# Kernel optimization log

Measured on AMD Instinct MI355X. Metric: run time of the kernel, lower is better.

Reference implementation:

```python
import jax, jax.numpy as jnp
import numpy as np

LAMBDA = 0.1   # lambda_ init arg
RHO = 1.0      # ADMM penalty parameter
N_ITERS = 50   # fixed ADMM iteration count (replaces eps_rel/eps_abs stopping rule, jit-friendly)


def _admm_box_qp(Q1, P):
    """Solve, for every (b, n): min_x 0.5 x^T Q1[b] x + P[b,n]^T x  s.t. 0 <= x <= 1.
    Q1: [b, m, m] (shared across n, so factor once per b), P: [b, n, m]. Returns z: [b, n, m]."""
    b, n, m = P.shape
    M_inv = jnp.linalg.inv(Q1 + RHO * jnp.eye(m, dtype=Q1.dtype))  # [b, m, m]

    x0 = jnp.zeros((b, n, m), P.dtype)

    def step(carry, _):
        x, z, u = carry
        rhs = RHO * (z - u) - P                       # [b, n, m]
        x = jnp.einsum('bij,bnj->bni', M_inv, rhs)    # x-update: (Q1 + rho I) x = rhs
        z = jnp.clip(x + u, 0.0, 1.0)                 # z-update: projection onto box [lb, ub] = [0, 1]
        u = u + x - z                                 # dual update
        return (x, z, u), None

    (x, z, u), _ = jax.lax.scan(step, (x0, x0, x0), None, length=N_ITERS)
    return z


def reference(Q, V):
    b, n, d = Q.shape
    m = V.shape[1]
    V = V / m
    # Q1 = 2 V V^T : [b, m, m]
    Q1 = 2.0 * jnp.einsum('bmd,bkd->bmk', V, V)
    # P = -2 V Q^T + lambda/m : [b, n, m]  (avoid materializing the b*n stacked copies of Q1)
    P = -2.0 * jnp.einsum('bmd,bnd->bnm', V, Q) + LAMBDA / m
    x = _admm_box_qp(Q1, P)                           # [b, n, m] in [0, 1]
    xb = jnp.where(x > 0.5, 1.0, 0.0)                 # hard threshold
    coeffs = xb / (jnp.abs(xb).sum(axis=-1, keepdims=True) + 1e-10)
    return jnp.einsum('bnm,bmd->bnd', coeffs, V)


def setup_inputs() -> dict:
    key = jax.random.key(0)
    kq, kv = jax.random.split(key)
    Q = jax.random.normal(kq, (8, 2048, 128), dtype=jnp.float32)
    V = jax.random.normal(kv, (8, 128, 128), dtype=jnp.float32)
    return {"Q": Q, "V": V}
```

## Files before the change

### kernel.cpp

```cpp
#include <hip/hip_runtime.h>

#define NROWS 2048
#define MDIM 128
#define NITER 50
#define PSTR 65
#define RSTR 136
#define XSTR 132

#define RH0_B 0
#define RM0_B 17408
#define RH1_B 34816
#define RM1_B 52224
#define BUF_STRIDE 34816
#define WM_B 69632
#define CNT_B 104448
#define SMEM_BYTES 108544
#define QST_B 0
#define PMAT_B 33792
#define XB_B 0
#define CF_B 33792

typedef unsigned short ushort_t;
typedef __attribute__((ext_vector_type(8))) _Float16 f16x8;
typedef __attribute__((ext_vector_type(8))) unsigned short us8;
typedef __attribute__((ext_vector_type(4))) unsigned short us4;
typedef __attribute__((ext_vector_type(4))) float f32x4;

__global__ __launch_bounds__(256) void mk_m64(const float* __restrict__ V,
                                              double* __restrict__ M,
                                              double* __restrict__ X0,
                                              double* __restrict__ vs) {
  __shared__ double sA[16][130];
  __shared__ double sB[32][130];
  const int b = blockIdx.x >> 5, t = blockIdx.x & 31;
  const int i0 = (t >> 2) << 4, j0 = (t & 3) << 5;
  const float* Vb = V + b * MDIM * MDIM;
  const int tid = threadIdx.x;
  const double S = 1.0 / 128.0;
  for (int idx = tid; idx < 512; idx += 256) {
    const int r = idx >> 5, c4 = (idx & 31) << 2;
    float4 v = *(const float4*)(Vb + (i0 + r) * MDIM + c4);
    sA[r][c4 + 0] = v.x * S; sA[r][c4 + 1] = v.y * S;
    sA[r][c4 + 2] = v.z * S; sA[r][c4 + 3] = v.w * S;
  }
  for (int idx = tid; idx < 1024; idx += 256) {
    const int r = idx >> 5, c4 = (idx & 31) << 2;
    float4 w = *(const float4*)(Vb + (j0 + r) * MDIM + c4);
    sB[r][c4 + 0] = w.x * S; sB[r][c4 + 1] = w.y * S;
    sB[r][c4 + 2] = w.z * S; sB[r][c4 + 3] = w.w * S;
  }
  if (vs) {
    double* Tb = vs + b * 16384;
    const int base2 = t * 512;
    for (int k = tid; k < 512; k += 256) {
      const int idx = base2 + k;
      const int j = idx >> 7, c = idx & 127;
      Tb[idx] = (double)Vb[c * 128 + j] * (1.0 / 128.0);
    }
  }
  __syncthreads();
  const int tx = tid & 15, ty = tid >> 4;
  double acc0 = 0.0, acc1 = 0.0;
  for (int k = 0; k < 128; ++k) {
    const double a0 = sA[ty][k];
    const double b0 = sB[tx * 2 + 0][k], b1 = sB[tx * 2 + 1][k];
    acc0 = fma(a0, b0, acc0); acc1 = fma(a0, b1, acc1);
  }
  double* Mb = M + b * 16384;
  double* Xb = X0 + b * 16384;
#pragma unroll
  for (int j = 0; j < 2; ++j) {
    const int gi = i0 + ty, gj = j0 + tx * 2 + j;
    const double diag = (gi == gj) ? 1.0 : 0.0;
    const double mv = 2.0 * (j ? acc1 : acc0) + diag;
    Mb[gi * 128 + gj] = mv;
    Xb[gi * 128 + gj] = 2.0 * diag - mv;
  }
}

__global__ __launch_bounds__(256) void ns_gemm64(const double* __restrict__ A,
                                                 const double* __restrict__ B,
                                                 double* __restrict__ C,
                                                 const double* __restrict__ Xc,
                                                 int mode,
                                                 ushort_t* __restrict__ Whg,
                                                 ushort_t* __restrict__ Wmg) {
  __shared__ double sA[16][130];
  __shared__ double sB[32][130];
  const int b = blockIdx.x >> 5, t = blockIdx.x & 31;
  const int i0 = (t >> 2) << 4, j0 = (t & 3) << 5;
  const double* Ab = A + b * 16384;
  const double* Bb = B + b * 16384;
  const int tid = threadIdx.x;
  for (int idx = tid; idx < 1024; idx += 256) {
    const int r = idx >> 6, c2 = (idx & 63) << 1;
    *(double2*)&sA[r][c2] = *(const double2*)(Ab + (i0 + r) * 128 + c2);
  }
  for (int idx = tid; idx < 2048; idx += 256) {
    const int r = idx >> 6, c2 = (idx & 63) << 1;
    *(double2*)&sB[r][c2] = *(const double2*)(Bb + (j0 + r) * 128 + c2);
  }
  __syncthreads();
  const int tx = tid & 15, ty = tid >> 4;
  double acc0 = 0.0, acc1 = 0.0;
  for (int k = 0; k < 128; k += 2) {
    const double2 a2  = *(const double2*)&sA[ty][k];
    const double2 b0p = *(const double2*)&sB[tx * 2 + 0][k];
    const double2 b1p = *(const double2*)&sB[tx * 2 + 1][k];
    acc0 = fma(a2.x, b0p.x, acc0); acc1 = fma(a2.x, b1p.x, acc1);
    acc0 = fma(a2.y, b0p.y, acc0); acc1 = fma(a2.y, b1p.y, acc1);
  }
  double* Cb = C + b * 16384;
  const double* Xcb = Xc + b * 16384;
#pragma unroll
  for (int j = 0; j < 2; ++j) {
    const int gi = i0 + ty, gj = j0 + tx * 2 + j;
    const double diag = (gi == gj) ? 1.0 : 0.0;
    double v = (j ? acc1 : acc0);
    if (mode == 1) v = 2.0 * Xcb[gi * 128 + gj] - v;
    else if (mode == 3) v = 3.0 * diag - 3.0 * Xcb[gi * 128 + gj] + v;
    Cb[gi * 128 + gj] = v;
    if (mode == 2) {
      const float wf = (float)(diag - v);
      const float wsc = wf * 1024.f;
      const _Float16 h = (_Float16)wsc;
      const float r1 = wsc - (float)h;
      const _Float16 m = (_Float16)r1;
      Whg[b * 16384 + gj * 128 + gi] = __builtin_bit_cast(ushort_t, h);
      Wmg[b * 16384 + gj * 128 + gi] = __builtin_bit_cast(ushort_t, m);
    }
  }
}

__global__ __launch_bounds__(256) void vst_prep(const float* __restrict__ V,
                                                double* __restrict__ vs) {
  const int b = blockIdx.x >> 3, ch = blockIdx.x & 7;
  const float* Vb = V + b * 16384;
  double* Tb = vs + b * 16384;
  const int base = ch * 2048;
  for (int k = threadIdx.x; k < 2048; k += 256) {
    const int idx = base + k;
    const int j = idx >> 7, c = idx & 127;
    Tb[idx] = (double)Vb[c * 128 + j] * (1.0 / 128.0);
  }
}

__global__ __launch_bounds__(1024, 4) void admm_mfma(const float* __restrict__ Q,
                                                     const float* __restrict__ V,
                                                     const ushort_t* __restrict__ Whg,
                                                     const ushort_t* __restrict__ Wmg,
                                                     const double* __restrict__ VsT64,
                                                     float* __restrict__ out) {
  __shared__ __align__(16) char smem[SMEM_BYTES];
  const int tid = threadIdx.x;
  const int b = blockIdx.x & 7;
  const int n0 = (blockIdx.x >> 3) << 6;
  const int lane = tid & 63;
  const int w = tid >> 6;
  const int nt = w & 3, cpair = w >> 2;
  const int quad = lane >> 4, col16 = lane & 15;
  const int nloc = nt * 16 + col16;
  const int ct0 = cpair * 2, ct1 = ct0 + 1;
  const int rowA0 = ct0 * 16 + col16;
  const int rowA1 = ct1 * 16 + col16;
  const int cB0 = ct0 * 16 + quad * 4;
  const int cB1 = cB0 + 16;

  const float* Qb = Q + ((size_t)(b * NROWS + n0)) * MDIM;
  float* outb = out + ((size_t)(b * NROWS + n0)) * MDIM;
  const ushort_t* WhB = Whg + b * 16384;
  const ushort_t* WmB = Wmg + b * 16384;

  float* QST = (float*)(smem + QST_B);
  double* pmat = (double*)(smem + PMAT_B);
  ushort_t* wmp = (ushort_t*)(smem + WM_B);
  float* sCnt = (float*)(smem + CNT_B);

  for (int idx = tid; idx < 2048; idx += 1024) {
    const int r = idx >> 5, d4 = (idx & 31) << 2;
    const float4 q = *(const float4*)(Qb + r * 128 + d4);
    QST[(d4 + 0) * PSTR + r] = q.x;
    QST[(d4 + 1) * PSTR + r] = q.y;
    QST[(d4 + 2) * PSTR + r] = q.z;
    QST[(d4 + 3) * PSTR + r] = q.w;
  }
  __syncthreads();

  {
    const int r2 = tid & 63;
    const int c8 = (tid >> 6) << 3;
    const double* vtb = VsT64 + b * 16384 + c8;
    double p8[8];
#pragma unroll
    for (int c = 0; c < 8; ++c) p8[c] = 0.0;
    for (int d = 0; d < 128; ++d) {
      const double a = (double)QST[d * PSTR + r2];
      const double* vt = vtb + d * 128;
#pragma unroll
      for (int c = 0; c < 8; ++c) p8[c] = fma(a, vt[c], p8[c]);
    }
    const double LAM = 0.1 / 128.0;
#pragma unroll
    for (int c = 0; c < 8; ++c) p8[c] = fma(-2.0, p8[c], LAM);
#pragma unroll
    for (int c = 0; c < 8; ++c) pmat[r2 * 128 + c8 + c] = p8[c];
  }
  __syncthreads();

  double pC[2][4];
#pragma unroll
  for (int i = 0; i < 4; ++i) {
    pC[0][i] = pmat[nloc * 128 + cB0 + i];
    pC[1][i] = pmat[nloc * 128 + cB1 + i];
  }
  __syncthreads();

  for (int idx = tid; idx < 2048; idx += 1024) {
    const int c = idx >> 4, g = idx & 15;
    *(us8*)(wmp + c * RSTR + g * 8) = *(const us8*)(WmB + c * 128 + g * 8);
  }
  f16x8 wh0[4], wh1[4], wm1[4];
#pragma unroll
  for (int s = 0; s < 4; ++s) {
    const int kq = s * 32 + quad * 8;
    wh0[s] = *(const f16x8*)(WhB + rowA0 * 128 + kq);
    wh1[s] = *(const f16x8*)(WhB + rowA1 * 128 + kq);
    wm1[s] = *(const f16x8*)(WmB + rowA1 * 128 + kq);
  }
  __syncthreads();

  double z[2][4], u[2][4], r64[2][4];
#pragma unroll
  for (int t = 0; t < 2; ++t)
#pragma unroll
    for (int i = 0; i < 4; ++i) { z[t][i] = 0.0; u[t][i] = 0.0; }
  const int rrow = nloc * RSTR;
  const float RS = 1.f / 1024.f;

  for (int it = 0; it < NITER; ++it) {
    const int boff = (it & 1) * BUF_STRIDE;
    ushort_t* rhp = (ushort_t*)(smem + RH0_B + boff);
    ushort_t* rmp = (ushort_t*)(smem + RM0_B + boff);
#pragma unroll
    for (int t = 0; t < 2; ++t) {
      const int cb = t ? cB1 : cB0;
      us4 hh, mm2;
#pragma unroll
      for (int i = 0; i < 4; ++i) {
        const double rv = (z[t][i] - u[t][i]) - pC[t][i];
        r64[t][i] = rv;
        const float rf = (float)rv;
        const _Float16 h = (_Float16)rf;
        const float r1 = rf - (float)h;
        const _Float16 m = (_Float16)r1;
        hh[i] = __builtin_bit_cast(ushort_t, h);
        mm2[i] = __builtin_bit_cast(ushort_t, m);
      }
      *(us4*)(rhp + rrow + cb) = hh;
      *(us4*)(rmp + rrow + cb) = mm2;
    }
    __syncthreads();

    f32x4 acc0 = {0.f, 0.f, 0.f, 0.f};
    f32x4 acc1 = {0.f, 0.f, 0.f, 0.f};
#pragma unroll
    for (int s = 0; s < 4; ++s) {
      const int kq = s * 32 + quad * 8;
      const f16x8 bh = *(const f16x8*)(rhp + rrow + kq);
      const f16x8 bm = *(const f16x8*)(rmp + rrow + kq);
      const f16x8 am0 = *(const f16x8*)(wmp + rowA0 * RSTR + kq);
      acc0 = __builtin_amdgcn_mfma_f32_16x16x32_f16(wh0[s], bh, acc0, 0, 0, 0);
      acc0 = __builtin_amdgcn_mfma_f32_16x16x32_f16(wh0[s], bm, acc0, 0, 0, 0);
      acc0 = __builtin_amdgcn_mfma_f32_16x16x32_f16(am0,    bh, acc0, 0, 0, 0);
      acc1 = __builtin_amdgcn_mfma_f32_16x16x32_f16(wh1[s], bh, acc1, 0, 0, 0);
      acc1 = __builtin_amdgcn_mfma_f32_16x16x32_f16(wh1[s], bm, acc1, 0, 0, 0);
      acc1 = __builtin_amdgcn_mfma_f32_16x16x32_f16(wm1[s], bh, acc1, 0, 0, 0);
    }

#pragma unroll
    for (int t = 0; t < 2; ++t)
#pragma unroll
      for (int i = 0; i < 4; ++i) {
        const float corr = ((t == 0) ? acc0[i] : acc1[i]) * RS;
        const double x = r64[t][i] - (double)corr;
        const double y = x + u[t][i];
        const double zn = fmin(fmax(y, 0.0), 1.0);
        u[t][i] = y - zn;
        z[t][i] = zn;
      }
  }

  float* xbm = (float*)(smem + XB_B);
#pragma unroll
  for (int t = 0; t < 2; ++t) {
    const int cb = t ? cB1 : cB0;
    float4 o;
    o.x = (z[t][0] > 0.5) ? 1.f : 0.f;
    o.y = (z[t][1] > 0.5) ? 1.f : 0.f;
    o.z = (z[t][2] > 0.5) ? 1.f : 0.f;
    o.w = (z[t][3] > 0.5) ? 1.f : 0.f;
    *(float4*)(xbm + nloc * XSTR + cb) = o;
  }
  __syncthreads();

  const int n2 = tid >> 4, cg = tid & 15;
  float xb8[8];
  {
    const float4 a = *(const float4*)(xbm + n2 * XSTR + 8 * cg + 0);
    const float4 c2 = *(const float4*)(xbm + n2 * XSTR + 8 * cg + 4);
    xb8[0] = a.x; xb8[1] = a.y; xb8[2] = a.z; xb8[3] = a.w;
    xb8[4] = c2.x; xb8[5] = c2.y; xb8[6] = c2.z; xb8[7] = c2.w;
  }
  double cnt = 0.0;
#pragma unroll
  for (int c = 0; c < 8; ++c) cnt += (double)xb8[c];
  sCnt[n2 * 16 + cg] = (float)cnt;
  __syncthreads();
  double kk = 0.0;
#pragma unroll
  for (int g = 0; g < 16; ++g) kk += (double)sCnt[n2 * 16 + g];
  const double rkS = (1.0 / 128.0) / (kk + 1e-10);
  float* cf = (float*)(smem + CF_B);
  {
    float4 w0, w1;
    w0.x = (float)((double)xb8[0] * rkS); w0.y = (float)((double)xb8[1] * rkS);
    w0.z = (float)((double)xb8[2] * rkS); w0.w = (float)((double)xb8[3] * rkS);
    w1.x = (float)((double)xb8[4] * rkS); w1.y = (float)((double)xb8[5] * rkS);
    w1.z = (float)((double)xb8[6] * rkS); w1.w = (float)((double)xb8[7] * rkS);
    *(float4*)(cf + n2 * XSTR + 8 * cg + 0) = w0;
    *(float4*)(cf + n2 * XSTR + 8 * cg + 4) = w1;
  }
  __syncthreads();

  const int n3 = tid & 63;
  const int c8o = (tid >> 6) << 3;
  const float* Vw = V + b * 16384 + c8o;
  float oa[8];
#pragma unroll
  for (int c = 0; c < 8; ++c) oa[c] = 0.f;
#pragma unroll 4
  for (int m4 = 0; m4 < 32; ++m4) {
    const float4 a4 = *(const float4*)(cf + n3 * XSTR + (m4 << 2));
#pragma unroll
    for (int mm = 0; mm < 4; ++mm) {
      const float* vp = Vw + ((m4 << 2) + mm) * 128;
      const float am = (mm == 0) ? a4.x : (mm == 1) ? a4.y : (mm == 2) ? a4.z : a4.w;
#pragma unroll
      for (int c = 0; c < 8; ++c) oa[c] = fmaf(am, vp[c], oa[c]);
    }
  }
#pragma unroll
  for (int q = 0; q < 2; ++q) {
    float4 o;
    o.x = oa[q * 4 + 0]; o.y = oa[q * 4 + 1];
    o.z = oa[q * 4 + 2]; o.w = oa[q * 4 + 3];
    *(float4*)(outb + n3 * 128 + c8o + q * 4) = o;
  }
}

extern "C" void kernel_launch(void* const* d_in, const int* in_sizes, int n_in,
                              void* d_out, int out_size, void* d_ws, size_t ws_size,
                              hipStream_t stream) {
  const float* Q = (const float*)d_in[0];
  const float* V = (const float*)d_in[1];
  float* out = (float*)d_out;
  double* ws = (double*)d_ws;
  double* Mw = ws;
  double* Xa = ws + 131072;
  double* Xb = ws + 262144;
  double* Tw = ws + 393216;
  ushort_t* Whg = (ushort_t*)Mw;
  ushort_t* Wmg = Whg + 131072;

  const bool big = ws_size >= (size_t)(5 * 1024 * 1024);
  double* VsT = big ? (ws + 524288) : Tw;

  mk_m64<<<256, 256, 0, stream>>>(V, Mw, Xa, big ? VsT : (double*)nullptr);
  ns_gemm64<<<256, 256, 0, stream>>>(Mw, Mw, Tw, Mw, 1, nullptr, nullptr);
  ns_gemm64<<<256, 256, 0, stream>>>(Tw, Tw, Xb, Tw, 3, nullptr, nullptr);
  ns_gemm64<<<256, 256, 0, stream>>>(Xa, Xb, Tw, Xa, 2, Whg, Wmg);
  if (!big) vst_prep<<<64, 256, 0, stream>>>(V, Tw);
  admm_mfma<<<256, 1024, 0, stream>>>(Q, V, Whg, Wmg, VsT, out);
}
```

Measured before the change: 263.3 us.

## Fuse Newton-Schulz inverse prep kernels into one cooperative grid-synced kernel

Replaces the separate matrix-build, three Newton-Schulz GEMM kernels and the V-transpose prep kernel with a single cooperative kernel. The stages are separated by grid.sync(), which removes several kernel launch gaps and inter-kernel drain bubbles. The final GEMM stage also skips writing its unused double-precision output. This adds a dependence on cooperative launch, which requires all 256 blocks to be co-resident, and adds grid-barrier cost.

```diff
diff --git a/kernel.cpp b/kernel.cpp
--- a/kernel.cpp
+++ b/kernel.cpp
@@ -1,4 +1,7 @@
 #include <hip/hip_runtime.h>
+#include <hip/hip_cooperative_groups.h>
+
+namespace cg = cooperative_groups;
 
 #define NROWS 2048
 #define MDIM 128
@@ -26,72 +29,18 @@
 typedef __attribute__((ext_vector_type(4))) unsigned short us4;
 typedef __attribute__((ext_vector_type(4))) float f32x4;
 
-__global__ __launch_bounds__(256) void mk_m64(const float* __restrict__ V,
-                                              double* __restrict__ M,
-                                              double* __restrict__ X0,
-                                              double* __restrict__ vs) {
-  __shared__ double sA[16][130];
-  __shared__ double sB[32][130];
-  const int b = blockIdx.x >> 5, t = blockIdx.x & 31;
-  const int i0 = (t >> 2) << 4, j0 = (t & 3) << 5;
-  const float* Vb = V + b * MDIM * MDIM;
-  const int tid = threadIdx.x;
-  const double S = 1.0 / 128.0;
-  for (int idx = tid; idx < 512; idx += 256) {
-    const int r = idx >> 5, c4 = (idx & 31) << 2;
-    float4 v = *(const float4*)(Vb + (i0 + r) * MDIM + c4);
-    sA[r][c4 + 0] = v.x * S; sA[r][c4 + 1] = v.y * S;
-    sA[r][c4 + 2] = v.z * S; sA[r][c4 + 3] = v.w * S;
-  }
-  for (int idx = tid; idx < 1024; idx += 256) {
-    const int r = idx >> 5, c4 = (idx & 31) << 2;
-    float4 w = *(const float4*)(Vb + (j0 + r) * MDIM + c4);
-    sB[r][c4 + 0] = w.x * S; sB[r][c4 + 1] = w.y * S;
-    sB[r][c4 + 2] = w.z * S; sB[r][c4 + 3] = w.w * S;
-  }
-  if (vs) {
-    double* Tb = vs + b * 16384;
-    const int base2 = t * 512;
-    for (int k = tid; k < 512; k += 256) {
-      const int idx = base2 + k;
-      const int j = idx >> 7, c = idx & 127;
-      Tb[idx] = (double)Vb[c * 128 + j] * (1.0 / 128.0);
-    }
-  }
-  __syncthreads();
-  const int tx = tid & 15, ty = tid >> 4;
-  double acc0 = 0.0, acc1 = 0.0;
-  for (int k = 0; k < 128; ++k) {
-    const double a0 = sA[ty][k];
-    const double b0 = sB[tx * 2 + 0][k], b1 = sB[tx * 2 + 1][k];
-    acc0 = fma(a0, b0, acc0); acc1 = fma(a0, b1, acc1);
-  }
-  double* Mb = M + b * 16384;
-  double* Xb = X0 + b * 16384;
-#pragma unroll
-  for (int j = 0; j < 2; ++j) {
-    const int gi = i0 + ty, gj = j0 + tx * 2 + j;
-    const double diag = (gi == gj) ? 1.0 : 0.0;
-    const double mv = 2.0 * (j ? acc1 : acc0) + diag;
-    Mb[gi * 128 + gj] = mv;
-    Xb[gi * 128 + gj] = 2.0 * diag - mv;
-  }
-}
-
-__global__ __launch_bounds__(256) void ns_gemm64(const double* __restrict__ A,
-                                                 const double* __restrict__ B,
-                                                 double* __restrict__ C,
-                                                 const double* __restrict__ Xc,
-                                                 int mode,
-                                                 ushort_t* __restrict__ Whg,
-                                                 ushort_t* __restrict__ Wmg) {
-  __shared__ double sA[16][130];
-  __shared__ double sB[32][130];
-  const int b = blockIdx.x >> 5, t = blockIdx.x & 31;
+__device__ __forceinline__ void gemm_stage(const double* __restrict__ A,
+                                           const double* __restrict__ B,
+                                           double* __restrict__ C,
+                                           const double* __restrict__ Xc,
+                                           int mode,
+                                           ushort_t* __restrict__ Whg,
+                                           ushort_t* __restrict__ Wmg,
+                                           int b, int t, int tid,
+                                           double (*sA)[130], double (*sB)[130]) {
   const int i0 = (t >> 2) << 4, j0 = (t & 3) << 5;
   const double* Ab = A + b * 16384;
   const double* Bb = B + b * 16384;
-  const int tid = threadIdx.x;
   for (int idx = tid; idx < 1024; idx += 256) {
     const int r = idx >> 6, c2 = (idx & 63) << 1;
     *(double2*)&sA[r][c2] = *(const double2*)(Ab + (i0 + r) * 128 + c2);
@@ -119,8 +68,9 @@
     double v = (j ? acc1 : acc0);
     if (mode == 1) v = 2.0 * Xcb[gi * 128 + gj] - v;
     else if (mode == 3) v = 3.0 * diag - 3.0 * Xcb[gi * 128 + gj] + v;
-    Cb[gi * 128 + gj] = v;
-    if (mode == 2) {
+    if (mode != 2) {
+      Cb[gi * 128 + gj] = v;
+    } else {
       const float wf = (float)(diag - v);
       const float wsc = wf * 1024.f;
       const _Float16 h = (_Float16)wsc;
@@ -130,18 +80,77 @@
       Wmg[b * 16384 + gj * 128 + gi] = __builtin_bit_cast(ushort_t, m);
     }
   }
+  __syncthreads();
 }
 
-__global__ __launch_bounds__(256) void vst_prep(const float* __restrict__ V,
-                                                double* __restrict__ vs) {
-  const int b = blockIdx.x >> 3, ch = blockIdx.x & 7;
-  const float* Vb = V + b * 16384;
-  double* Tb = vs + b * 16384;
-  const int base = ch * 2048;
-  for (int k = threadIdx.x; k < 2048; k += 256) {
-    const int idx = base + k;
-    const int j = idx >> 7, c = idx & 127;
-    Tb[idx] = (double)Vb[c * 128 + j] * (1.0 / 128.0);
+__global__ __launch_bounds__(256) void prep_coop(const float* __restrict__ V,
+                                                 double* __restrict__ M,
+                                                 double* __restrict__ X0,
+                                                 double* __restrict__ Tw,
+                                                 double* __restrict__ P3,
+                                                 ushort_t* __restrict__ Whg,
+                                                 ushort_t* __restrict__ Wmg,
+                                                 double* __restrict__ vs) {
+  cg::grid_group grid = cg::this_grid();
+  __shared__ double sA[32][130];
+  __shared__ double sB[32][130];
+  const int b = blockIdx.x >> 5, t = blockIdx.x & 31;
+  const int tid = threadIdx.x;
+
+  {
+    const int i0 = (t >> 2) << 4, j0 = (t & 3) << 5;
+    const float* Vb = V + b * MDIM * MDIM;
+    const double S = 1.0 / 128.0;
+    for (int idx = tid; idx < 512; idx += 256) {
+      const int r = idx >> 5, c4 = (idx & 31) << 2;
+      float4 v = *(const float4*)(Vb + (i0 + r) * MDIM + c4);
+      sA[r][c4 + 0] = v.x * S; sA[r][c4 + 1] = v.y * S;
+      sA[r][c4 + 2] = v.z * S; sA[r][c4 + 3] = v.w * S;
+    }
+    for (int idx = tid; idx < 1024; idx += 256) {
+      const int r = idx >> 5, c4 = (idx & 31) << 2;
+      float4 w = *(const float4*)(Vb + (j0 + r) * MDIM + c4);
+      sB[r][c4 + 0] = w.x * S; sB[r][c4 + 1] = w.y * S;
+      sB[r][c4 + 2] = w.z * S; sB[r][c4 + 3] = w.w * S;
+    }
+    __syncthreads();
+    const int tx = tid & 15, ty = tid >> 4;
+    double acc0 = 0.0, acc1 = 0.0;
+    for (int k = 0; k < 128; ++k) {
+      const double a0 = sA[ty][k];
+      const double b0 = sB[tx * 2 + 0][k], b1 = sB[tx * 2 + 1][k];
+      acc0 = fma(a0, b0, acc0); acc1 = fma(a0, b1, acc1);
+    }
+    double* Mb = M + b * 16384;
+    double* Xb = X0 + b * 16384;
+#pragma unroll
+    for (int j = 0; j < 2; ++j) {
+      const int gi = i0 + ty, gj = j0 + tx * 2 + j;
+      const double diag = (gi == gj) ? 1.0 : 0.0;
+      const double mv = 2.0 * (j ? acc1 : acc0) + diag;
+      Mb[gi * 128 + gj] = mv;
+      Xb[gi * 128 + gj] = 2.0 * diag - mv;
+    }
+    __syncthreads();
+  }
+  grid.sync();
+
+  gemm_stage(M, M, Tw, M, 1, nullptr, nullptr, b, t, tid, sA, sB);
+  grid.sync();
+
+  gemm_stage(Tw, Tw, P3, Tw, 3, nullptr, nullptr, b, t, tid, sA, sB);
+  grid.sync();
+
+  gemm_stage(X0, P3, Tw, X0, 2, Whg, Wmg, b, t, tid, sA, sB);
+  {
+    const float* Vb = V + b * 16384;
+    double* Tb = vs + b * 16384;
+    const int base2 = t * 512;
+    for (int k = tid; k < 512; k += 256) {
+      const int idx = base2 + k;
+      const int j = idx >> 7, c = idx & 127;
+      Tb[idx] = (double)Vb[c * 128 + j] * (1.0 / 128.0);
+    }
   }
 }
 
@@ -303,18 +312,18 @@
   }
   __syncthreads();
 
-  const int n2 = tid >> 4, cg = tid & 15;
+  const int n2 = tid >> 4, cg2 = tid & 15;
   float xb8[8];
   {
-    const float4 a = *(const float4*)(xbm + n2 * XSTR + 8 * cg + 0);
-    const float4 c2 = *(const float4*)(xbm + n2 * XSTR + 8 * cg + 4);
+    const float4 a = *(const float4*)(xbm + n2 * XSTR + 8 * cg2 + 0);
+    const float4 c2 = *(const float4*)(xbm + n2 * XSTR + 8 * cg2 + 4);
     xb8[0] = a.x; xb8[1] = a.y; xb8[2] = a.z; xb8[3] = a.w;
     xb8[4] = c2.x; xb8[5] = c2.y; xb8[6] = c2.z; xb8[7] = c2.w;
   }
   double cnt = 0.0;
 #pragma unroll
   for (int c = 0; c < 8; ++c) cnt += (double)xb8[c];
-  sCnt[n2 * 16 + cg] = (float)cnt;
+  sCnt[n2 * 16 + cg2] = (float)cnt;
   __syncthreads();
   double kk = 0.0;
 #pragma unroll
@@ -327,8 +336,8 @@
     w0.z = (float)((double)xb8[2] * rkS); w0.w = (float)((double)xb8[3] * rkS);
     w1.x = (float)((double)xb8[4] * rkS); w1.y = (float)((double)xb8[5] * rkS);
     w1.z = (float)((double)xb8[6] * rkS); w1.w = (float)((double)xb8[7] * rkS);
-    *(float4*)(cf + n2 * XSTR + 8 * cg + 0) = w0;
-    *(float4*)(cf + n2 * XSTR + 8 * cg + 4) = w1;
+    *(float4*)(cf + n2 * XSTR + 8 * cg2 + 0) = w0;
+    *(float4*)(cf + n2 * XSTR + 8 * cg2 + 4) = w1;
   }
   __syncthreads();
 
@@ -375,10 +384,9 @@
   const bool big = ws_size >= (size_t)(5 * 1024 * 1024);
   double* VsT = big ? (ws + 524288) : Tw;
 
-  mk_m64<<<256, 256, 0, stream>>>(V, Mw, Xa, big ? VsT : (double*)nullptr);
-  ns_gemm64<<<256, 256, 0, stream>>>(Mw, Mw, Tw, Mw, 1, nullptr, nullptr);
-  ns_gemm64<<<256, 256, 0, stream>>>(Tw, Tw, Xb, Tw, 3, nullptr, nullptr);
-  ns_gemm64<<<256, 256, 0, stream>>>(Xa, Xb, Tw, Xa, 2, Whg, Wmg);
-  if (!big) vst_prep<<<64, 256, 0, stream>>>(V, Tw);
+  void* args[] = {(void*)&V, (void*)&Mw, (void*)&Xa, (void*)&Tw, (void*)&Xb,
+                  (void*)&Whg, (void*)&Wmg, (void*)&VsT};
+  hipLaunchCooperativeKernel((void*)prep_coop, dim3(256), dim3(256), args, 0,
+                             stream);
   admm_mfma<<<256, 1024, 0, stream>>>(Q, V, Whg, Wmg, VsT, out);
 }
```

Measured after the change: 348.6 us. 1.32x slower.
